# Kernel optimization log

Measured on AMD Instinct MI355X. Metric: run time of the kernel, lower is better.

## Reference

```python
import jax, jax.numpy as jnp
import numpy as np

EPS = 1e-8


def _laplace_normalize(edge_row, edge_col, edge_vals, num_nodes):
    # D_r^{-1/2} A D_c^{-1/2} as in laplace_transform
    deg_r = jax.ops.segment_sum(edge_vals, edge_row, num_segments=num_nodes)
    deg_c = jax.ops.segment_sum(edge_vals, edge_col, num_segments=num_nodes)
    inv_r = 1.0 / (jnp.sqrt(deg_r) + EPS)
    inv_c = 1.0 / (jnp.sqrt(deg_c) + EPS)
    return edge_vals * inv_r[edge_row] * inv_c[edge_col]


def _l2norm(x):
    # F.normalize(p=2, dim=1): x / max(||x||, eps) with eps=1e-12
    n = jnp.sqrt(jnp.sum(x * x, axis=1, keepdims=True))
    return x / jnp.maximum(n, 1e-12)


def setup_inputs() -> dict:
    key = jax.random.key(0)
    k1, k2, k3, k4, k5, k6 = jax.random.split(key, 6)
    N, D, E, B = 100000, 64, 3200000, 4096
    node_features = jax.random.normal(k1, (N, D), dtype=jnp.float32)
    edge_row = jax.random.randint(k2, (E,), 0, N, dtype=jnp.int32)
    edge_col = jax.random.randint(k3, (E,), 0, N, dtype=jnp.int32)
    edge_vals = jnp.ones((E,), dtype=jnp.float32)
    a_id = jax.random.randint(k4, (B,), 0, N, dtype=jnp.int32)
    pos_id = jax.random.randint(k5, (B,), 0, N, dtype=jnp.int32)
    neg_id = jax.random.randint(k6, (B,), 0, N, dtype=jnp.int32)
    return {"node_features": node_features, "edge_row": edge_row,
            "edge_col": edge_col, "edge_vals": edge_vals,
            "a_id": a_id, "pos_id": pos_id, "neg_id": neg_id}


def reference(node_features, edge_row, edge_col, edge_vals, a_id, pos_id, neg_id):
    num_nodes = node_features.shape[0]
    num_layers = 3
    norm_vals = _laplace_normalize(edge_row, edge_col, edge_vals, num_nodes)

    # one_propagate: repeated spmm + per-layer L2 normalize, mean over layers
    features = node_features
    acc = node_features  # layer-0 term of the running sum (not normalized)
    for _ in range(num_layers):
        msgs = norm_vals[:, None] * features[edge_col]  # [E, D]
        features = jax.ops.segment_sum(msgs, edge_row, num_segments=num_nodes)
        acc = acc + _l2norm(features)
    node_rep = acc / (num_layers + 1)

    # BPR loss over batch
    a = node_rep[a_id]
    pos_pred = jnp.sum(a * node_rep[pos_id], axis=1)
    neg_pred = jnp.sum(a * node_rep[neg_id], axis=1)
    loss = jnp.mean(-jax.nn.log_sigmoid(pos_pred - neg_pred))
    return loss
```

## Files before the change

kernel.cpp:

```cpp
#include <hip/hip_runtime.h>
#include <math.h>

#define DDIM 64
#define BUCKET 256
#define LRSHIFT 17
#define CMASK 0x1FFFF
#define LRMASK 0xFF
#define NBLK 512
#define TPB_BIN 1024
#define NWV 16
#define MAXNB 400

typedef unsigned long long ull;
typedef _Float16 half2_t __attribute__((ext_vector_type(2)));

__device__ inline unsigned int bf16_hi(float v) {
    unsigned int a = __float_as_uint(v);
    return (a + 0x7fffu + ((a >> 16) & 1u)) & 0xffff0000u;
}

__device__ inline unsigned int pk_f16x2(float lo, float hi) {
    return __builtin_bit_cast(unsigned int, __builtin_amdgcn_cvt_pkrtz(lo, hi));
}

__device__ inline half2_t dup_lo16(unsigned int s) {
    return __builtin_bit_cast(half2_t, __builtin_amdgcn_perm(0u, s, 0x01000100u));
}

__device__ inline half2_t h2_shfl_xor(half2_t v, int off) {
    return __builtin_bit_cast(half2_t, __shfl_xor(__builtin_bit_cast(unsigned int, v), off));
}

__global__ void init_fill_kernel(int* __restrict__ gfill_r, int* __restrict__ gfill_c,
                                 int NB, int cap) {
    int k = blockIdx.x * blockDim.x + threadIdx.x;
    if (k < NB) {
        gfill_r[k * 16] = k * cap;
        gfill_c[k * 16] = k * cap;
    }
}

__global__ __launch_bounds__(TPB_BIN)
void binning_kernel(const int* __restrict__ erow, const int* __restrict__ ecol,
                    const float* __restrict__ evals,
                    int* __restrict__ gfill_r, int* __restrict__ gfill_c,
                    ull* __restrict__ br, unsigned int* __restrict__ bc,
                    int E, int NB, int chunk) {
    __shared__ int hr[NWV][MAXNB];
    __shared__ int hc[NWV][MAXNB];
    __shared__ int fr[MAXNB];
    __shared__ int fc[MAXNB];
    int t = threadIdx.x;
    int wv = t >> 6;
    for (int k = t; k < NWV * MAXNB; k += TPB_BIN) { (&hr[0][0])[k] = 0; (&hc[0][0])[k] = 0; }
    __syncthreads();
    int lo = blockIdx.x * chunk;
    int hi = min(E, lo + chunk);
    int nq = (hi - lo) >> 2;
    int rem = (hi - lo) & 3;
    int p0 = t, p1 = t + TPB_BIN;
    bool h0 = p0 < nq, h1 = p1 < nq;
    int4 r40, c40, r41, c41;
    float4 v40, v41;
    if (h0) {
        int i = lo + 4 * p0;
        r40 = *(const int4*)(erow + i);
        c40 = *(const int4*)(ecol + i);
        v40 = *(const float4*)(evals + i);
        atomicAdd(&hr[wv][r40.x >> 8], 1);
        atomicAdd(&hr[wv][r40.y >> 8], 1);
        atomicAdd(&hr[wv][r40.z >> 8], 1);
        atomicAdd(&hr[wv][r40.w >> 8], 1);
        atomicAdd(&hc[wv][c40.x >> 8], 1);
        atomicAdd(&hc[wv][c40.y >> 8], 1);
        atomicAdd(&hc[wv][c40.z >> 8], 1);
        atomicAdd(&hc[wv][c40.w >> 8], 1);
    }
    if (h1) {
        int i = lo + 4 * p1;
        r41 = *(const int4*)(erow + i);
        c41 = *(const int4*)(ecol + i);
        v41 = *(const float4*)(evals + i);
        atomicAdd(&hr[wv][r41.x >> 8], 1);
        atomicAdd(&hr[wv][r41.y >> 8], 1);
        atomicAdd(&hr[wv][r41.z >> 8], 1);
        atomicAdd(&hr[wv][r41.w >> 8], 1);
        atomicAdd(&hc[wv][c41.x >> 8], 1);
        atomicAdd(&hc[wv][c41.y >> 8], 1);
        atomicAdd(&hc[wv][c41.z >> 8], 1);
        atomicAdd(&hc[wv][c41.w >> 8], 1);
    }
    if (t == 0) {
        for (int i = hi - rem; i < hi; i++) {
            atomicAdd(&hr[0][erow[i] >> 8], 1);
            atomicAdd(&hc[0][ecol[i] >> 8], 1);
        }
    }
    __syncthreads();
    if (t < NB) {
        int sr = 0, sc = 0;
        #pragma unroll
        for (int w2 = 0; w2 < NWV; w2++) { sr += hr[w2][t]; sc += hc[w2][t]; }
        fr[t] = atomicAdd(&gfill_r[t * 16], sr);
        fc[t] = atomicAdd(&gfill_c[t * 16], sc);
    }
    __syncthreads();
    if (h0) {
        int pos0 = atomicAdd(&fr[r40.x >> 8], 1);
        int pos1 = atomicAdd(&fr[r40.y >> 8], 1);
        int pos2 = atomicAdd(&fr[r40.z >> 8], 1);
        int pos3 = atomicAdd(&fr[r40.w >> 8], 1);
        br[pos0] = ((ull)__float_as_uint(v40.x) << 32) | ((ull)(r40.x & 255) << LRSHIFT) | (unsigned)c40.x;
        br[pos1] = ((ull)__float_as_uint(v40.y) << 32) | ((ull)(r40.y & 255) << LRSHIFT) | (unsigned)c40.y;
        br[pos2] = ((ull)__float_as_uint(v40.z) << 32) | ((ull)(r40.z & 255) << LRSHIFT) | (unsigned)c40.z;
        br[pos3] = ((ull)__float_as_uint(v40.w) << 32) | ((ull)(r40.w & 255) << LRSHIFT) | (unsigned)c40.w;
        int q0 = atomicAdd(&fc[c40.x >> 8], 1);
        int q1 = atomicAdd(&fc[c40.y >> 8], 1);
        int q2 = atomicAdd(&fc[c40.z >> 8], 1);
        int q3 = atomicAdd(&fc[c40.w >> 8], 1);
        bc[q0] = bf16_hi(v40.x) | (unsigned)(c40.x & 255);
        bc[q1] = bf16_hi(v40.y) | (unsigned)(c40.y & 255);
        bc[q2] = bf16_hi(v40.z) | (unsigned)(c40.z & 255);
        bc[q3] = bf16_hi(v40.w) | (unsigned)(c40.w & 255);
    }
    if (h1) {
        int pos0 = atomicAdd(&fr[r41.x >> 8], 1);
        int pos1 = atomicAdd(&fr[r41.y >> 8], 1);
        int pos2 = atomicAdd(&fr[r41.z >> 8], 1);
        int pos3 = atomicAdd(&fr[r41.w >> 8], 1);
        br[pos0] = ((ull)__float_as_uint(v41.x) << 32) | ((ull)(r41.x & 255) << LRSHIFT) | (unsigned)c41.x;
        br[pos1] = ((ull)__float_as_uint(v41.y) << 32) | ((ull)(r41.y & 255) << LRSHIFT) | (unsigned)c41.y;
        br[pos2] = ((ull)__float_as_uint(v41.z) << 32) | ((ull)(r41.z & 255) << LRSHIFT) | (unsigned)c41.z;
        br[pos3] = ((ull)__float_as_uint(v41.w) << 32) | ((ull)(r41.w & 255) << LRSHIFT) | (unsigned)c41.w;
        int q0 = atomicAdd(&fc[c41.x >> 8], 1);
        int q1 = atomicAdd(&fc[c41.y >> 8], 1);
        int q2 = atomicAdd(&fc[c41.z >> 8], 1);
        int q3 = atomicAdd(&fc[c41.w >> 8], 1);
        bc[q0] = bf16_hi(v41.x) | (unsigned)(c41.x & 255);
        bc[q1] = bf16_hi(v41.y) | (unsigned)(c41.y & 255);
        bc[q2] = bf16_hi(v41.z) | (unsigned)(c41.z & 255);
        bc[q3] = bf16_hi(v41.w) | (unsigned)(c41.w & 255);
    }
    if (t == 0) {
        for (int i = hi - rem; i < hi; i++) {
            int r = erow[i], c = ecol[i];
            float v = evals[i];
            int pos = atomicAdd(&fr[r >> 8], 1);
            br[pos] = ((ull)__float_as_uint(v) << 32) | ((ull)(r & 255) << LRSHIFT) | (unsigned)c;
            int pos2 = atomicAdd(&fc[c >> 8], 1);
            bc[pos2] = bf16_hi(v) | (unsigned)(c & 255);
        }
    }
}

__global__ __launch_bounds__(BUCKET)
void fused_cp_kernel(const ull* __restrict__ br, const unsigned int* __restrict__ bc,
                     const int* __restrict__ gfill_r, const int* __restrict__ gfill_c,
                     int2* __restrict__ rse, float* __restrict__ inv_c,
                     unsigned int* __restrict__ cw, int N, int cap) {
    __shared__ int   cnt[BUCKET];
    __shared__ float ds[BUCKET];
    __shared__ float dsc[BUCKET];
    __shared__ int   sc[BUCKET];
    __shared__ float invr[BUCKET];
    int b = blockIdx.x, t = threadIdx.x;
    cnt[t] = 0; ds[t] = 0.0f; dsc[t] = 0.0f;
    __syncthreads();
    int s = b * cap;
    int e = gfill_r[b * 16];
    int m = s + ((e - s) & ~3);
    for (int i = s + 4 * t; i < m; i += 4 * BUCKET) {
        ull p0 = br[i];
        ull p1 = br[i + 1];
        ull p2 = br[i + 2];
        ull p3 = br[i + 3];
        int lr0 = (int)((p0 >> LRSHIFT) & LRMASK);
        int lr1 = (int)((p1 >> LRSHIFT) & LRMASK);
        int lr2 = (int)((p2 >> LRSHIFT) & LRMASK);
        int lr3 = (int)((p3 >> LRSHIFT) & LRMASK);
        atomicAdd(&cnt[lr0], 1);
        atomicAdd(&cnt[lr1], 1);
        atomicAdd(&cnt[lr2], 1);
        atomicAdd(&cnt[lr3], 1);
        atomicAdd(&ds[lr0], __uint_as_float((unsigned)(p0 >> 32)));
        atomicAdd(&ds[lr1], __uint_as_float((unsigned)(p1 >> 32)));
        atomicAdd(&ds[lr2], __uint_as_float((unsigned)(p2 >> 32)));
        atomicAdd(&ds[lr3], __uint_as_float((unsigned)(p3 >> 32)));
    }
    if (t == 0) {
        for (int i = m; i < e; i++) {
            ull p = br[i];
            int lr = (int)((p >> LRSHIFT) & LRMASK);
            atomicAdd(&cnt[lr], 1);
            atomicAdd(&ds[lr], __uint_as_float((unsigned)(p >> 32)));
        }
    }
    int e2 = gfill_c[b * 16];
    int m2 = s + ((e2 - s) & ~3);
    for (int i = s + 4 * t; i < m2; i += 4 * BUCKET) {
        uint4 p = *(const uint4*)(bc + i);
        atomicAdd(&dsc[p.x & 0xFFu], __uint_as_float(p.x & 0xffff0000u));
        atomicAdd(&dsc[p.y & 0xFFu], __uint_as_float(p.y & 0xffff0000u));
        atomicAdd(&dsc[p.z & 0xFFu], __uint_as_float(p.z & 0xffff0000u));
        atomicAdd(&dsc[p.w & 0xFFu], __uint_as_float(p.w & 0xffff0000u));
    }
    if (t == 0) {
        for (int i = m2; i < e2; i++) {
            unsigned int p = bc[i];
            atomicAdd(&dsc[p & 0xFFu], __uint_as_float(p & 0xffff0000u));
        }
    }
    __syncthreads();
    int c0 = cnt[t];
    int sum4 = (c0 + 3) & ~3;
    sc[t] = sum4;
    __syncthreads();
    for (int off = 1; off < BUCKET; off <<= 1) {
        int v = (t >= off) ? sc[t - off] : 0;
        __syncthreads();
        sc[t] += v;
        __syncthreads();
    }
    int st = s + sc[t] - sum4;
    int node = b * BUCKET + t;
    if (node < N) {
        int2 se;
        se.x = st;
        se.y = st + c0;
        rse[node] = se;
    }
    inv_c[node] = 1.0f / (sqrtf(dsc[t]) + 1e-8f);
    invr[t] = 1.0f / (sqrtf(ds[t]) + 1e-8f);
    cnt[t] = st;
    __syncthreads();
    for (int i = s + 4 * t; i < m; i += 4 * BUCKET) {
        ull p0 = br[i];
        ull p1 = br[i + 1];
        ull p2 = br[i + 2];
        ull p3 = br[i + 3];
        int c0_ = (int)(p0 & CMASK), c1_ = (int)(p1 & CMASK);
        int c2_ = (int)(p2 & CMASK), c3_ = (int)(p3 & CMASK);
        int lr0 = (int)((p0 >> LRSHIFT) & LRMASK);
        int lr1 = (int)((p1 >> LRSHIFT) & LRMASK);
        int lr2 = (int)((p2 >> LRSHIFT) & LRMASK);
        int lr3 = (int)((p3 >> LRSHIFT) & LRMASK);
        float v0 = __uint_as_float((unsigned)(p0 >> 32));
        float v1 = __uint_as_float((unsigned)(p1 >> 32));
        float v2 = __uint_as_float((unsigned)(p2 >> 32));
        float v3 = __uint_as_float((unsigned)(p3 >> 32));
        int pos0 = atomicAdd(&cnt[lr0], 1);
        int pos1 = atomicAdd(&cnt[lr1], 1);
        int pos2 = atomicAdd(&cnt[lr2], 1);
        int pos3 = atomicAdd(&cnt[lr3], 1);
        float w0 = v0 * invr[lr0];
        float w1 = v1 * invr[lr1];
        float w2 = v2 * invr[lr2];
        float w3 = v3 * invr[lr3];
        cw[pos0] = ((unsigned)c0_ << 15) | ((pk_f16x2(w0, w0) & 0xFFFFu) >> 1);
        cw[pos1] = ((unsigned)c1_ << 15) | ((pk_f16x2(w1, w1) & 0xFFFFu) >> 1);
        cw[pos2] = ((unsigned)c2_ << 15) | ((pk_f16x2(w2, w2) & 0xFFFFu) >> 1);
        cw[pos3] = ((unsigned)c3_ << 15) | ((pk_f16x2(w3, w3) & 0xFFFFu) >> 1);
    }
    if (t == 0) {
        for (int i = m; i < e; i++) {
            ull p = br[i];
            int c = (int)(p & CMASK);
            int lr = (int)((p >> LRSHIFT) & LRMASK);
            float v = __uint_as_float((unsigned)(p >> 32));
            int pos = atomicAdd(&cnt[lr], 1);
            float wv = v * invr[lr];
            cw[pos] = ((unsigned)c << 15) | ((pk_f16x2(wv, wv) & 0xFFFFu) >> 1);
        }
    }
}

__global__ void cvt_kernel(const float* __restrict__ src, const float* __restrict__ inv_c,
                           unsigned int* __restrict__ dst, long n4) {
    long i = (long)blockIdx.x * blockDim.x + threadIdx.x;
    if (i < n4) {
        float ic = inv_c[i >> 4];
        float4 v = ((const float4*)src)[i];
        uint2 o;
        o.x = pk_f16x2(v.x * ic, v.y * ic);
        o.y = pk_f16x2(v.z * ic, v.w * ic);
        ((uint2*)dst)[i] = o;
    }
}

__global__ __launch_bounds__(256)
void spmm_f16_kernel(const int2* __restrict__ rse,
                     const unsigned int* __restrict__ cw,
                     const float* __restrict__ inv_c,
                     const unsigned short* __restrict__ fin,
                     unsigned short* __restrict__ fout, int N) {
    int wid = blockIdx.x * (blockDim.x >> 6) + (threadIdx.x >> 6);
    if (wid >= N) return;
    int lane = threadIdx.x & 63;
    int g = lane >> 3;
    int h = lane & 7;
    int2 se = rse[wid];
    float ic = inv_c[wid];
    int s = se.x, e = se.y;
    half2_t a2[8];
    #pragma unroll
    for (int k = 0; k < 8; k++) a2[k] = (half2_t)0;

    for (int base = s; base < e; base += 32) {
        int j = base + 4 * g;
        if (j < e) {
            uint4 pw = *(const uint4*)(cw + j);
            int c0 = (int)(pw.x >> 15);
            int c1 = (j + 1 < e) ? (int)(pw.y >> 15) : c0;
            int c2 = (j + 2 < e) ? (int)(pw.z >> 15) : c0;
            int c3 = (j + 3 < e) ? (int)(pw.w >> 15) : c0;
            uint4 q0 = ((const uint4*)(fin + ((long)c0 << 6)))[h];
            uint4 q1 = ((const uint4*)(fin + ((long)c1 << 6)))[h];
            uint4 q2 = ((const uint4*)(fin + ((long)c2 << 6)))[h];
            uint4 q3 = ((const uint4*)(fin + ((long)c3 << 6)))[h];
            half2_t w0 = dup_lo16(pw.x << 1);
            half2_t w1 = (j + 1 < e) ? dup_lo16(pw.y << 1) : (half2_t)0;
            half2_t w2 = (j + 2 < e) ? dup_lo16(pw.z << 1) : (half2_t)0;
            half2_t w3 = (j + 3 < e) ? dup_lo16(pw.w << 1) : (half2_t)0;
            a2[0] += w0 * __builtin_bit_cast(half2_t, q0.x);
            a2[1] += w0 * __builtin_bit_cast(half2_t, q0.y);
            a2[2] += w0 * __builtin_bit_cast(half2_t, q0.z);
            a2[3] += w0 * __builtin_bit_cast(half2_t, q0.w);
            a2[4] += w1 * __builtin_bit_cast(half2_t, q1.x);
            a2[5] += w1 * __builtin_bit_cast(half2_t, q1.y);
            a2[6] += w1 * __builtin_bit_cast(half2_t, q1.z);
            a2[7] += w1 * __builtin_bit_cast(half2_t, q1.w);
            a2[0] += w2 * __builtin_bit_cast(half2_t, q2.x);
            a2[1] += w2 * __builtin_bit_cast(half2_t, q2.y);
            a2[2] += w2 * __builtin_bit_cast(half2_t, q2.z);
            a2[3] += w2 * __builtin_bit_cast(half2_t, q2.w);
            a2[4] += w3 * __builtin_bit_cast(half2_t, q3.x);
            a2[5] += w3 * __builtin_bit_cast(half2_t, q3.y);
            a2[6] += w3 * __builtin_bit_cast(half2_t, q3.z);
            a2[7] += w3 * __builtin_bit_cast(half2_t, q3.w);
        }
    }

    #pragma unroll
    for (int k = 0; k < 4; k++) a2[k] += a2[k + 4];
    #pragma unroll
    for (int k = 0; k < 4; k++) {
        a2[k] += h2_shfl_xor(a2[k], 8);
        a2[k] += h2_shfl_xor(a2[k], 16);
        a2[k] += h2_shfl_xor(a2[k], 32);
    }
    if (g == 0) {
        half2_t ich = __builtin_bit_cast(half2_t, pk_f16x2(ic, ic));
        uint4 o;
        o.x = __builtin_bit_cast(unsigned int, a2[0] * ich);
        o.y = __builtin_bit_cast(unsigned int, a2[1] * ich);
        o.z = __builtin_bit_cast(unsigned int, a2[2] * ich);
        o.w = __builtin_bit_cast(unsigned int, a2[3] * ich);
        ((uint4*)(fout + ((long)wid << 6)))[h] = o;
    }
}

__device__ inline float rep_at(const float* __restrict__ nf,
                               const unsigned short* __restrict__ f1,
                               const unsigned short* __restrict__ f2,
                               const unsigned short* __restrict__ f3,
                               int id, int lane) {
    long off = (long)id * DDIM + lane;
    float r  = nf[off];
    float v1 = (float)__builtin_bit_cast(_Float16, f1[off]);
    float v2 = (float)__builtin_bit_cast(_Float16, f2[off]);
    float v3 = (float)__builtin_bit_cast(_Float16, f3[off]);
    float s1 = v1 * v1, s2 = v2 * v2, s3 = v3 * v3;
    #pragma unroll
    for (int o = 1; o < 64; o <<= 1) {
        s1 += __shfl_xor(s1, o);
        s2 += __shfl_xor(s2, o);
        s3 += __shfl_xor(s3, o);
    }
    r += v1 / fmaxf(sqrtf(s1), 1e-12f);
    r += v2 / fmaxf(sqrtf(s2), 1e-12f);
    r += v3 / fmaxf(sqrtf(s3), 1e-12f);
    return r;
}

__global__ void loss_terms_kernel(const float* __restrict__ nf,
                                  const unsigned short* __restrict__ f1,
                                  const unsigned short* __restrict__ f2,
                                  const unsigned short* __restrict__ f3,
                                  const int* __restrict__ a_id, const int* __restrict__ p_id,
                                  const int* __restrict__ n_id,
                                  float* __restrict__ terms, int B) {
    long gid = (long)blockIdx.x * blockDim.x + threadIdx.x;
    int b = (int)(gid >> 6);
    int lane = threadIdx.x & 63;
    if (b < B) {
        float ra = rep_at(nf, f1, f2, f3, a_id[b], lane);
        float rp = rep_at(nf, f1, f2, f3, p_id[b], lane);
        float rn = rep_at(nf, f1, f2, f3, n_id[b], lane);
        float dp = ra * rp, dn = ra * rn;
        #pragma unroll
        for (int off = 1; off < 64; off <<= 1) { dp += __shfl_xor(dp, off); dn += __shfl_xor(dn, off); }
        if (lane == 0) {
            float x = (dp - dn) * 0.0625f;
            terms[b] = fmaxf(-x, 0.0f) + log1pf(expf(-fabsf(x)));
        }
    }
}

__global__ void reduce_kernel(const float* __restrict__ terms, float* __restrict__ out, int B) {
    __shared__ float sm[256];
    float s = 0.0f;
    for (int i = threadIdx.x; i < B; i += 256) s += terms[i];
    sm[threadIdx.x] = s;
    __syncthreads();
    for (int stride = 128; stride > 0; stride >>= 1) {
        if (threadIdx.x < stride) sm[threadIdx.x] += sm[threadIdx.x + stride];
        __syncthreads();
    }
    if (threadIdx.x == 0) out[0] = sm[0] / (float)B;
}

extern "C" void kernel_launch(void* const* d_in, const int* in_sizes, int n_in,
                              void* d_out, int out_size, void* d_ws, size_t ws_size,
                              hipStream_t stream) {
    const float* nf    = (const float*)d_in[0];
    const int*   erow  = (const int*)d_in[1];
    const int*   ecol  = (const int*)d_in[2];
    const float* evals = (const float*)d_in[3];
    const int*   a_id  = (const int*)d_in[4];
    const int*   p_id  = (const int*)d_in[5];
    const int*   n_id  = (const int*)d_in[6];

    int N = in_sizes[0] / DDIM;
    int E = in_sizes[1];
    int B = in_sizes[4];
    int NB = (N + BUCKET - 1) / BUCKET;
    int chunk = (((E + NBLK - 1) / NBLK) + 3) & ~3;
    int Npad = NB * BUCKET;

    long capl = ((long)E * BUCKET) / N;
    int cap = (int)(capl + capl / 8 + 2048);
    cap = (cap + 63) & ~63;

    size_t regionA = (size_t)cap * NB * 8;
    size_t regionB = (size_t)cap * NB * 4;
    size_t featB16 = (size_t)N * DDIM * 2;
    if (regionA < 2 * featB16) regionA = 2 * featB16;

    char* w = (char*)d_ws;
    ull*  br     = (ull*)w;
    char* regAp  = w;                 w += regionA;
    unsigned int* bc = (unsigned int*)w;
    unsigned int* cw = (unsigned int*)w;  w += regionB + 256;
    unsigned short* fb2 = (unsigned short*)w;  w += featB16;
    float* inv_c = (float*)w;         w += (size_t)Npad * 4;
    int2* rse    = (int2*)w;          w += (size_t)N * 8;
    int* gfill_r = (int*)w;           w += (size_t)NB * 16 * 4;
    int* gfill_c = (int*)w;           w += (size_t)NB * 16 * 4;
    float* terms = (float*)w;         w += (size_t)B * 4;

    unsigned short* fb0 = (unsigned short*)regAp;
    unsigned short* fb1 = (unsigned short*)(regAp + featB16);

    init_fill_kernel<<<(unsigned)((NB + 127) / 128), 128, 0, stream>>>(gfill_r, gfill_c, NB, cap);
    binning_kernel<<<NBLK, TPB_BIN, 0, stream>>>(erow, ecol, evals, gfill_r, gfill_c,
                                                 br, bc, E, NB, chunk);
    fused_cp_kernel<<<NB, BUCKET, 0, stream>>>(br, bc, gfill_r, gfill_c,
                                               rse, inv_c, cw, N, cap);

    long n4 = (long)N * DDIM / 4;
    cvt_kernel<<<(unsigned)((n4 + 255) / 256), 256, 0, stream>>>(nf, inv_c, (unsigned int*)fb0, n4);

    unsigned spmmGrid = (unsigned)((N + 3) / 4);
    spmm_f16_kernel<<<spmmGrid, 256, 0, stream>>>(rse, cw, inv_c, fb0, fb1, N);
    spmm_f16_kernel<<<spmmGrid, 256, 0, stream>>>(rse, cw, inv_c, fb1, fb2, N);
    spmm_f16_kernel<<<spmmGrid, 256, 0, stream>>>(rse, cw, inv_c, fb2, fb0, N);

    loss_terms_kernel<<<(unsigned)(((long)B * 64 + 255) / 256), 256, 0, stream>>>(
        nf, fb1, fb2, fb0, a_id, p_id, n_id, terms, B);
    reduce_kernel<<<1, 256, 0, stream>>>(terms, (float*)d_out, B);
}
```

Before: 367.5 us.

## Widen bucket-build block to 1024 threads and size binning grid by chunk cap

The binning kernel now derives its grid size from a fixed maximum chunk of 12288 edges and handles up to three int4 groups per thread, which gives 261 blocks instead of 512 for this input. The per-bucket count/prefix/scatter kernel now runs 1024 threads per bucket instead of 256, so each bucket's ~8k edges are streamed by more threads. A separate cursor array replaces reuse of the count array. The aim is more parallelism and latency hiding in the preprocessing, at the cost of more LDS atomic contention and idle threads during the 256-wide scan.

```diff
diff --git a/kernel.cpp b/kernel.cpp
--- a/kernel.cpp
+++ b/kernel.cpp
@@ -6,10 +6,10 @@
 #define LRSHIFT 17
 #define CMASK 0x1FFFF
 #define LRMASK 0xFF
-#define NBLK 512
 #define TPB_BIN 1024
 #define NWV 16
 #define MAXNB 400
+#define CHUNKMAX 12288
 
 typedef unsigned long long ull;
 typedef _Float16 half2_t __attribute__((ext_vector_type(2)));
@@ -58,10 +58,10 @@
     int hi = min(E, lo + chunk);
     int nq = (hi - lo) >> 2;
     int rem = (hi - lo) & 3;
-    int p0 = t, p1 = t + TPB_BIN;
-    bool h0 = p0 < nq, h1 = p1 < nq;
-    int4 r40, c40, r41, c41;
-    float4 v40, v41;
+    int p0 = t, p1 = t + TPB_BIN, p2 = t + 2 * TPB_BIN;
+    bool h0 = p0 < nq, h1 = p1 < nq, h2 = p2 < nq;
+    int4 r40, c40, r41, c41, r42, c42;
+    float4 v40, v41, v42;
     if (h0) {
         int i = lo + 4 * p0;
         r40 = *(const int4*)(erow + i);
@@ -89,6 +89,20 @@
         atomicAdd(&hc[wv][c41.y >> 8], 1);
         atomicAdd(&hc[wv][c41.z >> 8], 1);
         atomicAdd(&hc[wv][c41.w >> 8], 1);
+    }
+    if (h2) {
+        int i = lo + 4 * p2;
+        r42 = *(const int4*)(erow + i);
+        c42 = *(const int4*)(ecol + i);
+        v42 = *(const float4*)(evals + i);
+        atomicAdd(&hr[wv][r42.x >> 8], 1);
+        atomicAdd(&hr[wv][r42.y >> 8], 1);
+        atomicAdd(&hr[wv][r42.z >> 8], 1);
+        atomicAdd(&hr[wv][r42.w >> 8], 1);
+        atomicAdd(&hc[wv][c42.x >> 8], 1);
+        atomicAdd(&hc[wv][c42.y >> 8], 1);
+        atomicAdd(&hc[wv][c42.z >> 8], 1);
+        atomicAdd(&hc[wv][c42.w >> 8], 1);
     }
     if (t == 0) {
         for (int i = hi - rem; i < hi; i++) {
@@ -141,6 +155,24 @@
         bc[q2] = bf16_hi(v41.z) | (unsigned)(c41.z & 255);
         bc[q3] = bf16_hi(v41.w) | (unsigned)(c41.w & 255);
     }
+    if (h2) {
+        int pos0 = atomicAdd(&fr[r42.x >> 8], 1);
+        int pos1 = atomicAdd(&fr[r42.y >> 8], 1);
+        int pos2 = atomicAdd(&fr[r42.z >> 8], 1);
+        int pos3 = atomicAdd(&fr[r42.w >> 8], 1);
+        br[pos0] = ((ull)__float_as_uint(v42.x) << 32) | ((ull)(r42.x & 255) << LRSHIFT) | (unsigned)c42.x;
+        br[pos1] = ((ull)__float_as_uint(v42.y) << 32) | ((ull)(r42.y & 255) << LRSHIFT) | (unsigned)c42.y;
+        br[pos2] = ((ull)__float_as_uint(v42.z) << 32) | ((ull)(r42.z & 255) << LRSHIFT) | (unsigned)c42.z;
+        br[pos3] = ((ull)__float_as_uint(v42.w) << 32) | ((ull)(r42.w & 255) << LRSHIFT) | (unsigned)c42.w;
+        int q0 = atomicAdd(&fc[c42.x >> 8], 1);
+        int q1 = atomicAdd(&fc[c42.y >> 8], 1);
+        int q2 = atomicAdd(&fc[c42.z >> 8], 1);
+        int q3 = atomicAdd(&fc[c42.w >> 8], 1);
+        bc[q0] = bf16_hi(v42.x) | (unsigned)(c42.x & 255);
+        bc[q1] = bf16_hi(v42.y) | (unsigned)(c42.y & 255);
+        bc[q2] = bf16_hi(v42.z) | (unsigned)(c42.z & 255);
+        bc[q3] = bf16_hi(v42.w) | (unsigned)(c42.w & 255);
+    }
     if (t == 0) {
         for (int i = hi - rem; i < hi; i++) {
             int r = erow[i], c = ecol[i];
@@ -153,23 +185,24 @@
     }
 }
 
-__global__ __launch_bounds__(BUCKET)
+__global__ __launch_bounds__(1024)
 void fused_cp_kernel(const ull* __restrict__ br, const unsigned int* __restrict__ bc,
                      const int* __restrict__ gfill_r, const int* __restrict__ gfill_c,
                      int2* __restrict__ rse, float* __restrict__ inv_c,
                      unsigned int* __restrict__ cw, int N, int cap) {
     __shared__ int   cnt[BUCKET];
+    __shared__ int   sc[BUCKET];
     __shared__ float ds[BUCKET];
     __shared__ float dsc[BUCKET];
-    __shared__ int   sc[BUCKET];
     __shared__ float invr[BUCKET];
+    __shared__ int   cur[BUCKET];
     int b = blockIdx.x, t = threadIdx.x;
-    cnt[t] = 0; ds[t] = 0.0f; dsc[t] = 0.0f;
+    if (t < BUCKET) { cnt[t] = 0; ds[t] = 0.0f; dsc[t] = 0.0f; }
     __syncthreads();
     int s = b * cap;
     int e = gfill_r[b * 16];
     int m = s + ((e - s) & ~3);
-    for (int i = s + 4 * t; i < m; i += 4 * BUCKET) {
+    for (int i = s + 4 * t; i < m; i += 4 * 1024) {
         ull p0 = br[i];
         ull p1 = br[i + 1];
         ull p2 = br[i + 2];
@@ -197,7 +230,7 @@
     }
     int e2 = gfill_c[b * 16];
     int m2 = s + ((e2 - s) & ~3);
-    for (int i = s + 4 * t; i < m2; i += 4 * BUCKET) {
+    for (int i = s + 4 * t; i < m2; i += 4 * 1024) {
         uint4 p = *(const uint4*)(bc + i);
         atomicAdd(&dsc[p.x & 0xFFu], __uint_as_float(p.x & 0xffff0000u));
         atomicAdd(&dsc[p.y & 0xFFu], __uint_as_float(p.y & 0xffff0000u));
@@ -211,65 +244,63 @@
         }
     }
     __syncthreads();
-    int c0 = cnt[t];
-    int sum4 = (c0 + 3) & ~3;
-    sc[t] = sum4;
+    int c0v = 0, sum4 = 0;
+    if (t < BUCKET) {
+        c0v = cnt[t];
+        sum4 = (c0v + 3) & ~3;
+        sc[t] = sum4;
+    }
     __syncthreads();
     for (int off = 1; off < BUCKET; off <<= 1) {
-        int v = (t >= off) ? sc[t - off] : 0;
+        int v = 0;
+        if (t >= off && t < BUCKET) v = sc[t - off];
         __syncthreads();
-        sc[t] += v;
+        if (t < BUCKET) sc[t] += v;
         __syncthreads();
     }
-    int st = s + sc[t] - sum4;
-    int node = b * BUCKET + t;
-    if (node < N) {
-        int2 se;
-        se.x = st;
-        se.y = st + c0;
-        rse[node] = se;
-    }
-    inv_c[node] = 1.0f / (sqrtf(dsc[t]) + 1e-8f);
-    invr[t] = 1.0f / (sqrtf(ds[t]) + 1e-8f);
-    cnt[t] = st;
-    __syncthreads();
-    for (int i = s + 4 * t; i < m; i += 4 * BUCKET) {
+    if (t < BUCKET) {
+        int st = s + sc[t] - sum4;
+        int node = b * BUCKET + t;
+        if (node < N) {
+            int2 se;
+            se.x = st;
+            se.y = st + c0v;
+            rse[node] = se;
+        }
+        inv_c[node] = 1.0f / (sqrtf(dsc[t]) + 1e-8f);
+        invr[t] = 1.0f / (sqrtf(ds[t]) + 1e-8f);
+        cur[t] = st;
+    }
+    __syncthreads();
+    for (int i = s + 4 * t; i < m; i += 4 * 1024) {
         ull p0 = br[i];
         ull p1 = br[i + 1];
         ull p2 = br[i + 2];
         ull p3 = br[i + 3];
-        int c0_ = (int)(p0 & CMASK), c1_ = (int)(p1 & CMASK);
-        int c2_ = (int)(p2 & CMASK), c3_ = (int)(p3 & CMASK);
         int lr0 = (int)((p0 >> LRSHIFT) & LRMASK);
         int lr1 = (int)((p1 >> LRSHIFT) & LRMASK);
         int lr2 = (int)((p2 >> LRSHIFT) & LRMASK);
         int lr3 = (int)((p3 >> LRSHIFT) & LRMASK);
-        float v0 = __uint_as_float((unsigned)(p0 >> 32));
-        float v1 = __uint_as_float((unsigned)(p1 >> 32));
-        float v2 = __uint_as_float((unsigned)(p2 >> 32));
-        float v3 = __uint_as_float((unsigned)(p3 >> 32));
-        int pos0 = atomicAdd(&cnt[lr0], 1);
-        int pos1 = atomicAdd(&cnt[lr1], 1);
-        int pos2 = atomicAdd(&cnt[lr2], 1);
-        int pos3 = atomicAdd(&cnt[lr3], 1);
-        float w0 = v0 * invr[lr0];
-        float w1 = v1 * invr[lr1];
-        float w2 = v2 * invr[lr2];
-        float w3 = v3 * invr[lr3];
-        cw[pos0] = ((unsigned)c0_ << 15) | ((pk_f16x2(w0, w0) & 0xFFFFu) >> 1);
-        cw[pos1] = ((unsigned)c1_ << 15) | ((pk_f16x2(w1, w1) & 0xFFFFu) >> 1);
-        cw[pos2] = ((unsigned)c2_ << 15) | ((pk_f16x2(w2, w2) & 0xFFFFu) >> 1);
-        cw[pos3] = ((unsigned)c3_ << 15) | ((pk_f16x2(w3, w3) & 0xFFFFu) >> 1);
+        int pos0 = atomicAdd(&cur[lr0], 1);
+        int pos1 = atomicAdd(&cur[lr1], 1);
+        int pos2 = atomicAdd(&cur[lr2], 1);
+        int pos3 = atomicAdd(&cur[lr3], 1);
+        float w0 = __uint_as_float((unsigned)(p0 >> 32)) * invr[lr0];
+        float w1 = __uint_as_float((unsigned)(p1 >> 32)) * invr[lr1];
+        float w2 = __uint_as_float((unsigned)(p2 >> 32)) * invr[lr2];
+        float w3 = __uint_as_float((unsigned)(p3 >> 32)) * invr[lr3];
+        cw[pos0] = ((unsigned)(p0 & CMASK) << 15) | ((pk_f16x2(w0, w0) & 0xFFFFu) >> 1);
+        cw[pos1] = ((unsigned)(p1 & CMASK) << 15) | ((pk_f16x2(w1, w1) & 0xFFFFu) >> 1);
+        cw[pos2] = ((unsigned)(p2 & CMASK) << 15) | ((pk_f16x2(w2, w2) & 0xFFFFu) >> 1);
+        cw[pos3] = ((unsigned)(p3 & CMASK) << 15) | ((pk_f16x2(w3, w3) & 0xFFFFu) >> 1);
     }
     if (t == 0) {
         for (int i = m; i < e; i++) {
             ull p = br[i];
-            int c = (int)(p & CMASK);
             int lr = (int)((p >> LRSHIFT) & LRMASK);
-            float v = __uint_as_float((unsigned)(p >> 32));
-            int pos = atomicAdd(&cnt[lr], 1);
-            float wv = v * invr[lr];
-            cw[pos] = ((unsigned)c << 15) | ((pk_f16x2(wv, wv) & 0xFFFFu) >> 1);
+            int pos = atomicAdd(&cur[lr], 1);
+            float wv = __uint_as_float((unsigned)(p >> 32)) * invr[lr];
+            cw[pos] = ((unsigned)(p & CMASK) << 15) | ((pk_f16x2(wv, wv) & 0xFFFFu) >> 1);
         }
     }
 }
@@ -434,6 +465,7 @@
     int E = in_sizes[1];
     int B = in_sizes[4];
     int NB = (N + BUCKET - 1) / BUCKET;
+    int NBLK = (E + CHUNKMAX - 1) / CHUNKMAX;
     int chunk = (((E + NBLK - 1) / NBLK) + 3) & ~3;
     int Npad = NB * BUCKET;
 
@@ -462,10 +494,10 @@
     unsigned short* fb1 = (unsigned short*)(regAp + featB16);
 
     init_fill_kernel<<<(unsigned)((NB + 127) / 128), 128, 0, stream>>>(gfill_r, gfill_c, NB, cap);
-    binning_kernel<<<NBLK, TPB_BIN, 0, stream>>>(erow, ecol, evals, gfill_r, gfill_c,
-                                                 br, bc, E, NB, chunk);
-    fused_cp_kernel<<<NB, BUCKET, 0, stream>>>(br, bc, gfill_r, gfill_c,
-                                               rse, inv_c, cw, N, cap);
+    binning_kernel<<<(unsigned)NBLK, TPB_BIN, 0, stream>>>(erow, ecol, evals, gfill_r, gfill_c,
+                                                           br, bc, E, NB, chunk);
+    fused_cp_kernel<<<(unsigned)NB, 1024, 0, stream>>>(br, bc, gfill_r, gfill_c,
+                                                       rse, inv_c, cw, N, cap);
 
     long n4 = (long)N * DDIM / 4;
     cvt_kernel<<<(unsigned)((n4 + 255) / 256), 256, 0, stream>>>(nf, inv_c, (unsigned int*)fb0, n4);
```

New measurement: 380.2 us. 3.5% more time.
